# Performance work log

Measured on AMD Instinct MI355X. Metric: run time of the kernel, lower is better.

Reference implementation:

```python
import jax, jax.numpy as jnp
import numpy as np
import math

B, T, D, H = 2, 2048, 768, 12
ND = D // H  # head dim = 64


def precompute_freqs_cis(dim, end, theta=10000.0):
    freqs = 1.0 / (theta ** (jnp.arange(0, dim, 2, dtype=jnp.float32) / dim))  # [dim/2]
    t = jnp.arange(end, dtype=jnp.float32)
    freqs = jnp.outer(t, freqs)  # [end, dim/2]
    return jnp.cos(freqs), jnp.sin(freqs)


def apply_rotary_emb(q, k, cos, sin):
    # q, k: [b, t, h, nd]; cos/sin: [t, nd/2]
    def rot(x):
        xr, xi = x[..., 0::2], x[..., 1::2]  # even/odd interleaved split
        c = cos[None, :, None, :]
        s = sin[None, :, None, :]
        out_r = xr * c - xi * s
        out_i = xr * s + xi * c
        return jnp.stack([out_r, out_i], axis=-1).reshape(x.shape)
    return rot(q), rot(k)


def setup_inputs() -> dict:
    key = jax.random.key(0)
    ks = jax.random.split(key, 12)
    sc = 0.02
    q = jax.random.normal(ks[0], (B, T, D), dtype=jnp.float32)
    k = jax.random.normal(ks[1], (B, T, D), dtype=jnp.float32)
    v = jax.random.normal(ks[2], (B, T, D), dtype=jnp.float32)
    mask = jnp.tril(jnp.ones((T, T), dtype=jnp.int32))[None, None]  # causal [1,1,T,T]
    # weights stored as [d_in, d_out] (pre-transposed vs torch Linear)
    wq = jax.random.normal(ks[3], (D, D), dtype=jnp.float32) * sc
    bq = jax.random.normal(ks[4], (D,), dtype=jnp.float32) * sc
    wk = jax.random.normal(ks[5], (D, D), dtype=jnp.float32) * sc
    bk = jax.random.normal(ks[6], (D,), dtype=jnp.float32) * sc
    wv = jax.random.normal(ks[7], (D, D), dtype=jnp.float32) * sc
    bv = jax.random.normal(ks[8], (D,), dtype=jnp.float32) * sc
    wo = jax.random.normal(ks[9], (D, D), dtype=jnp.float32) * sc
    cos, sin = precompute_freqs_cis(ND, T)
    return {"q": q, "k": k, "v": v, "mask": mask, "wq": wq, "bq": bq,
            "wk": wk, "bk": bk, "wv": wv, "bv": bv, "wo": wo,
            "freqs_cos": cos, "freqs_sin": sin}


def reference(q, k, v, mask, wq, bq, wk, bk, wv, bv, wo, freqs_cos, freqs_sin):
    b, t, d = q.shape
    qh = (q @ wq + bq).reshape(b, t, H, ND)
    kh = (k @ wk + bk).reshape(b, t, H, ND)
    vh = (v @ wv + bv).reshape(b, t, H, ND).transpose(0, 2, 1, 3)  # [b,h,t,nd]
    qh, kh = apply_rotary_emb(qh, kh, freqs_cos[:t], freqs_sin[:t])
    qh = qh.transpose(0, 2, 1, 3)  # [b,h,t,nd]
    kh = kh.transpose(0, 2, 1, 3)
    attn = jnp.einsum('bhqd,bhkd->bhqk', qh, kh) / math.sqrt(ND)
    attn = jnp.where(mask == 0, jnp.float32(-jnp.inf), attn)
    probs = jax.nn.softmax(attn, axis=-1)
    out = jnp.einsum('bhqk,bhkd->bhqd', probs, vh)
    out = out.transpose(0, 2, 1, 3).reshape(b, t, d)
    return out @ wo
```

## Files before the change

kernel.cpp:

```cpp
#include <hip/hip_runtime.h>
#include <hip/hip_bf16.h>
#include <math.h>

#define BB 2
#define TT 2048
#define DD 768
#define HH 12
#define ND 64
#define MM (BB*TT)

typedef __attribute__((ext_vector_type(8))) short bf16x8;
typedef __attribute__((ext_vector_type(4))) float f32x4;
typedef __attribute__((ext_vector_type(16))) float f32x16;

__device__ __forceinline__ float bf2f(ushort u) {
    union { unsigned int i; float f; } v; v.i = ((unsigned int)u) << 16; return v.f;
}
__device__ __forceinline__ ushort f2bf(float f) {
    union { float f; unsigned int i; } v; v.f = f;
    unsigned int r = v.i + 0x7FFF + ((v.i >> 16) & 1);
    return (ushort)(r >> 16);
}

__device__ __forceinline__ void cp16(void* lds, const void* g) {
    __builtin_amdgcn_global_load_lds(
        (const __attribute__((address_space(1))) void*)g,
        (__attribute__((address_space(3))) void*)lds, 16, 0, 0);
}

__device__ __forceinline__ float fexp2(float x) {
    float r; asm("v_exp_f32 %0, %1" : "=v"(r) : "v"(x)); return r;
}
__device__ __forceinline__ unsigned int pk_bf16(float a, float b) {
    unsigned int r; asm("v_cvt_pk_bf16_f32 %0, %1, %2" : "=v"(r) : "v"(a), "v"(b)); return r;
}

__device__ __forceinline__ void plswap(unsigned int& a, unsigned int& b) {
#if __has_builtin(__builtin_amdgcn_permlane32_swap)
    auto r = __builtin_amdgcn_permlane32_swap(a, b, false, false);
    a = r[0]; b = r[1];
#else
    unsigned int sa = __shfl_xor((int)a, 32), sb = __shfl_xor((int)b, 32);
    bool hi = (threadIdx.x & 63) >= 32;
    unsigned int na = hi ? sb : a, nb = hi ? b : sa;
    a = na; b = nb;
#endif
}
__device__ __forceinline__ float partner32(float x, int hi) {
#if __has_builtin(__builtin_amdgcn_permlane32_swap)
    unsigned int u = __float_as_uint(x);
    auto r = __builtin_amdgcn_permlane32_swap(u, u, false, false);
    return __uint_as_float(hi ? r[0] : r[1]);
#else
    return __shfl_xor(x, 32);
#endif
}

#define QSCALE 0.18033688011112043f

__global__ void conv_x3(const float* __restrict__ x0, const float* __restrict__ x1,
                        const float* __restrict__ x2,
                        ushort* __restrict__ o0, ushort* __restrict__ o1,
                        ushort* __restrict__ o2)
{
    const float* x = blockIdx.z == 0 ? x0 : (blockIdx.z == 1 ? x1 : x2);
    ushort* o = blockIdx.z == 0 ? o0 : (blockIdx.z == 1 ? o1 : o2);
    int i = (blockIdx.x * 256 + threadIdx.x) * 4;
    if (i >= MM * DD) return;
    float4 v = *(const float4*)&x[i];
    ushort4 r;
    r.x = f2bf(v.x); r.y = f2bf(v.y); r.z = f2bf(v.z); r.w = f2bf(v.w);
    *(ushort4*)&o[i] = r;
}

__global__ __launch_bounds__(256) void conv_wT(const float* __restrict__ w0, const float* __restrict__ w1,
                        const float* __restrict__ w2, const float* __restrict__ w3,
                        ushort* __restrict__ o0, ushort* __restrict__ o1,
                        ushort* __restrict__ o2, ushort* __restrict__ o3)
{
    __shared__ ushort tile[64][72];
    const float* w = blockIdx.z == 0 ? w0 : blockIdx.z == 1 ? w1 : blockIdx.z == 2 ? w2 : w3;
    ushort* o = blockIdx.z == 0 ? o0 : blockIdx.z == 1 ? o1 : blockIdx.z == 2 ? o2 : o3;
    const int k0 = blockIdx.y * 64, n0 = blockIdx.x * 64;
    #pragma unroll
    for (int it = 0; it < 4; ++it) {
        int e = (threadIdx.x + it * 256) * 4;
        int r = e >> 6, c = e & 63;
        float4 v = *(const float4*)&w[(size_t)(k0 + r) * DD + n0 + c];
        tile[c + 0][r] = f2bf(v.x);
        tile[c + 1][r] = f2bf(v.y);
        tile[c + 2][r] = f2bf(v.z);
        tile[c + 3][r] = f2bf(v.w);
    }
    __syncthreads();
    #pragma unroll
    for (int it = 0; it < 4; ++it) {
        int e = (threadIdx.x + it * 256) * 4;
        int nr = e >> 6, kc = e & 63;
        ushort4 r4;
        r4.x = tile[nr][kc + 0];
        r4.y = tile[nr][kc + 1];
        r4.z = tile[nr][kc + 2];
        r4.w = tile[nr][kc + 3];
        *(ushort4*)&o[(size_t)(n0 + nr) * DD + k0 + kc] = r4;
    }
}

struct GArgs { const ushort* x; const ushort* wt; const float* bias; void* out;
               const float* cT; const float* sT; int rope; };

template<int MODE, int TM, int TN>
__global__ __launch_bounds__(256) void gemm_bf16(GArgs a0, GArgs a1, GArgs a2)
{
    constexpr int WM = TM / 2, WN = TN / 2;
    constexpr int MF = WM / 16, NF = WN / 16;
    constexpr int BUFB = (TM + TN) * 64;
    constexpr int NPASS = BUFB / 4096;
    __shared__ __align__(16) ushort S[2][BUFB / 2];
    GArgs ga = (blockIdx.z == 0) ? a0 : (blockIdx.z == 1 ? a1 : a2);
    const int tid = threadIdx.x;
    const int w = tid >> 6, l = tid & 63;
    const int wr = w >> 1, wc = w & 1;
    const int n0 = blockIdx.x * TN, m0 = blockIdx.y * TM;

    f32x4 acc[MF][NF] = {};

    auto stage = [&](int buf, int k0) {
        #pragma unroll
        for (int it = 0; it < NPASS; ++it) {
            const int ob = it * 4096 + w * 1024;
            const int o = ob + l * 16;
            if (ob < TM * 64) {
                const int row = o >> 6, kb = o & 63;
                cp16((char*)&S[buf][0] + ob,
                     (const char*)ga.x + (size_t)(m0 + row) * (DD * 2) + k0 * 2 + kb);
            } else {
                const int o2 = o - TM * 64;
                const int row = o2 >> 6, kb = o2 & 63;
                cp16((char*)&S[buf][0] + ob,
                     (const char*)ga.wt + (size_t)(n0 + row) * (DD * 2) + k0 * 2 + kb);
            }
        }
    };
    stage(0, 0);
    __syncthreads();
    const int NK = DD / 32;
    for (int t = 0; t < NK; ++t) {
        const int cur = t & 1;
        if (t + 1 < NK) stage(cur ^ 1, (t + 1) * 32);
        const char* ab = (const char*)&S[cur][0];
        bf16x8 af[MF], bfr[NF];
        #pragma unroll
        for (int i = 0; i < MF; ++i)
            af[i] = *(const bf16x8*)(ab + (WM * wr + 16 * i + (l & 15)) * 64 + (l >> 4) * 16);
        #pragma unroll
        for (int j = 0; j < NF; ++j)
            bfr[j] = *(const bf16x8*)(ab + TM * 64 + (WN * wc + 16 * j + (l & 15)) * 64 + (l >> 4) * 16);
        #pragma unroll
        for (int i = 0; i < MF; ++i)
            #pragma unroll
            for (int j = 0; j < NF; ++j)
                acc[i][j] = __builtin_amdgcn_mfma_f32_16x16x32_bf16(af[i], bfr[j], acc[i][j], 0, 0, 0);
        __syncthreads();
    }
    #pragma unroll
    for (int i = 0; i < MF; ++i) {
        #pragma unroll
        for (int j = 0; j < NF; ++j) {
            #pragma unroll
            for (int r = 0; r < 4; ++r) {
                const int m = m0 + WM * wr + 16 * i + (l >> 4) * 4 + r;
                const int n = n0 + WN * wc + 16 * j + (l & 15);
                float v = acc[i][j][r];
                if (MODE == 0) {
                    v += ga.bias[n];
                    const int tt = m & 2047;
                    if (ga.rope) {
                        const int d = n & 63;
                        const float c = ga.cT[tt * 32 + (d >> 1)];
                        const float s = ga.sT[tt * 32 + (d >> 1)];
                        const float p = __shfl_xor(v, 1);
                        v = (n & 1) ? (p * s + v * c) : (v * c - p * s);
                        if (ga.rope == 2) v *= QSCALE;
                    }
                    const int b = m >> 11;
                    const int h = n >> 6, d = n & 63;
                    ((ushort*)ga.out)[((size_t)(b * HH + h) * TT + tt) * ND + d] = f2bf(v);
                } else {
                    ((float*)ga.out)[(size_t)m * DD + n] = v;
                }
            }
        }
    }
}

__global__ __launch_bounds__(256) void transpose_v(const ushort* __restrict__ Vh,
                                                   ushort* __restrict__ VhT)
{
    __shared__ ushort tile[64][72];
    const int t0 = blockIdx.x * 64, bh = blockIdx.y;
    const ushort* src = Vh + ((size_t)bh * TT + t0) * ND;
    #pragma unroll
    for (int it = 0; it < 4; ++it) {
        int e = (threadIdx.x + it * 256) * 4;
        int r = e >> 6, c = e & 63;
        ushort4 v = *(const ushort4*)&src[r * ND + c];
        tile[r][c + 0] = v.x; tile[r][c + 1] = v.y;
        tile[r][c + 2] = v.z; tile[r][c + 3] = v.w;
    }
    __syncthreads();
    #pragma unroll
    for (int it = 0; it < 4; ++it) {
        int e = (threadIdx.x + it * 256) * 4;
        int d = e >> 6, tc = e & 63;
        ushort4 r4;
        r4.x = tile[tc + 0][d]; r4.y = tile[tc + 1][d];
        r4.z = tile[tc + 2][d]; r4.w = tile[tc + 3][d];
        *(ushort4*)&VhT[((size_t)bh * ND + d) * TT + t0 + tc] = r4;
    }
}

#define NQB (TT/128)
#define NBH (BB*HH)
#define NTASK (NQB*NBH)
#define NCU 256

__global__ __launch_bounds__(512) void attn_mfma4(const ushort* __restrict__ Qh,
                                                  const ushort* __restrict__ Kh,
                                                  const ushort* __restrict__ VhT,
                                                  ushort* __restrict__ Op)
{
    __shared__ __align__(16) ushort Ks[2][2][4096];
    __shared__ __align__(16) ushort Vs[2][2][4096];
    const int tid = threadIdx.x;
    const int w = tid >> 6, l = tid & 63;
    const int lq = l & 31, hi = l >> 5;
    const int qs = w & 3;
    const int kvh = w >> 2;

    const int n = blockIdx.x;
    const int r_ = (n < NCU) ? n : (NTASK - 1 + NCU - n);
    const int qblk = (NQB - 1) - r_ / NBH;
    const int bh = r_ % NBH;

    const int q0 = qblk * 128;
    const int q0w = q0 + qs * 32;
    const int qg = q0w + lq;
    const int ntH = qblk + 1;
    const int kvbase = kvh * ntH * 64;

    const ushort* Qg = Qh + ((size_t)bh * TT + q0w) * ND;
    const ushort* Kg = Kh + (size_t)bh * TT * ND;
    const ushort* Vg = VhT + (size_t)bh * ND * TT;

    bf16x8 qf[4];
    #pragma unroll
    for (int ks = 0; ks < 4; ++ks)
        qf[ks] = *(const bf16x8*)((const char*)Qg + lq * 128 + ks * 32 + hi * 16);

    auto stageKV = [&](int buf, int kv0) {
        #pragma unroll
        for (int it = 0; it < 2; ++it) {
            int o = it * 4096 + qs * 1024 + l * 16;
            int row = o >> 7, inner = o & 127;
            int swz = inner ^ ((row & 7) << 4);
            cp16((char*)&Ks[kvh][buf][0] + it * 4096 + qs * 1024,
                 (const char*)Kg + (size_t)(kv0 + row) * 128 + swz);
            cp16((char*)&Vs[kvh][buf][0] + it * 4096 + qs * 1024,
                 (const char*)Vg + (size_t)row * (TT * 2) + kv0 * 2 + swz);
        }
    };

    float m = -1e30f, lsum = 0.f;
    f32x16 o0 = {}, o1 = {};

    stageKV(0, kvbase);
    __syncthreads();
    for (int t = 0; t < ntH; ++t) {
        const int cur = t & 1;
        if (t + 1 < ntH) stageKV(cur ^ 1, kvbase + (t + 1) * 64);
        const char* kb = (const char*)&Ks[kvh][cur][0];
        const char* vb = (const char*)&Vs[kvh][cur][0];
        const int kvt = kvbase + t * 64;

        if (kvt <= q0w + 31) {
            const bool have1 = (kvt + 32 <= q0w + 31);

            f32x16 st0 = {}, st1 = {};
            __builtin_amdgcn_s_setprio(1);
            #pragma unroll
            for (int ks = 0; ks < 4; ++ks) {
                bf16x8 kf = *(const bf16x8*)(kb + lq * 128 +
                                             ((ks * 32 + hi * 16) ^ ((lq & 7) << 4)));
                st0 = __builtin_amdgcn_mfma_f32_32x32x16_bf16(kf, qf[ks], st0, 0, 0, 0);
            }
            if (have1) {
                #pragma unroll
                for (int ks = 0; ks < 4; ++ks) {
                    bf16x8 kf = *(const bf16x8*)(kb + (32 + lq) * 128 +
                                                 ((ks * 32 + hi * 16) ^ ((lq & 7) << 4)));
                    st1 = __builtin_amdgcn_mfma_f32_32x32x16_bf16(kf, qf[ks], st1, 0, 0, 0);
                }
            }
            __builtin_amdgcn_s_setprio(0);

            float tm = -1e30f;
            if (kvt + 31 > q0w) {
                #pragma unroll
                for (int r = 0; r < 16; ++r) {
                    const int kvg = kvt + (r & 3) + 8 * (r >> 2) + 4 * hi;
                    float x = (kvg <= qg) ? st0[r] : -1e30f;
                    st0[r] = x;
                    tm = fmaxf(tm, x);
                }
            } else {
                #pragma unroll
                for (int r = 0; r < 16; ++r) tm = fmaxf(tm, st0[r]);
            }
            if (have1) {
                if (kvt + 63 > q0w) {
                    #pragma unroll
                    for (int r = 0; r < 16; ++r) {
                        const int kvg = kvt + 32 + (r & 3) + 8 * (r >> 2) + 4 * hi;
                        float x = (kvg <= qg) ? st1[r] : -1e30f;
                        st1[r] = x;
                        tm = fmaxf(tm, x);
                    }
                } else {
                    #pragma unroll
                    for (int r = 0; r < 16; ++r) tm = fmaxf(tm, st1[r]);
                }
            }
            tm = fmaxf(tm, partner32(tm, hi));

            const bool defer = __all(tm <= m + 11.5f);
            float alpha = 1.f;
            if (!defer) {
                const float nm = fmaxf(m, tm);
                alpha = fexp2(m - nm);
                m = nm;
            }

            float ps[16];
            unsigned int pkA[8], pkB[8];
            #pragma unroll
            for (int i = 0; i < 8; ++i) {
                const float p0 = fexp2(st0[2 * i + 0] - m);
                const float p1 = fexp2(st0[2 * i + 1] - m);
                pkA[i] = pk_bf16(p0, p1);
                ps[i] = p0 + p1;
            }
            if (have1) {
                #pragma unroll
                for (int i = 0; i < 8; ++i) {
                    const float p0 = fexp2(st1[2 * i + 0] - m);
                    const float p1 = fexp2(st1[2 * i + 1] - m);
                    pkB[i] = pk_bf16(p0, p1);
                    ps[8 + i] = p0 + p1;
                }
            } else {
                #pragma unroll
                for (int i = 0; i < 8; ++i) { pkB[i] = 0; ps[8 + i] = 0.f; }
            }
            const float t0s = (ps[0] + ps[1]) + (ps[2] + ps[3]);
            const float t1s = (ps[4] + ps[5]) + (ps[6] + ps[7]);
            const float t2s = (ps[8] + ps[9]) + (ps[10] + ps[11]);
            const float t3s = (ps[12] + ps[13]) + (ps[14] + ps[15]);
            float rs = (t0s + t1s) + (t2s + t3s);
            rs += partner32(rs, hi);
            lsum = lsum * alpha + rs;

            plswap(pkA[0], pkA[2]); plswap(pkA[1], pkA[3]);
            plswap(pkA[4], pkA[6]); plswap(pkA[5], pkA[7]);
            if (have1) {
                plswap(pkB[0], pkB[2]); plswap(pkB[1], pkB[3]);
                plswap(pkB[4], pkB[6]); plswap(pkB[5], pkB[7]);
            }
            union { unsigned int u[4]; bf16x8 v; } pa0, pa1, pa2, pa3;
            pa0.u[0] = pkA[0]; pa0.u[1] = pkA[1]; pa0.u[2] = pkA[2]; pa0.u[3] = pkA[3];
            pa1.u[0] = pkA[4]; pa1.u[1] = pkA[5]; pa1.u[2] = pkA[6]; pa1.u[3] = pkA[7];
            pa2.u[0] = pkB[0]; pa2.u[1] = pkB[1]; pa2.u[2] = pkB[2]; pa2.u[3] = pkB[3];
            pa3.u[0] = pkB[4]; pa3.u[1] = pkB[5]; pa3.u[2] = pkB[6]; pa3.u[3] = pkB[7];

            if (!defer) {
                #pragma unroll
                for (int r = 0; r < 16; ++r) { o0[r] *= alpha; o1[r] *= alpha; }
            }

            __builtin_amdgcn_s_setprio(1);
            #pragma unroll
            for (int sl = 0; sl < 2; ++sl) {
                const bf16x8 pf = sl == 0 ? pa0.v : pa1.v;
                const int cb = sl * 32 + hi * 16;
                bf16x8 va = *(const bf16x8*)(vb + lq * 128 + (cb ^ ((lq & 7) << 4)));
                bf16x8 vc = *(const bf16x8*)(vb + (lq + 32) * 128 + (cb ^ ((lq & 7) << 4)));
                o0 = __builtin_amdgcn_mfma_f32_32x32x16_bf16(va, pf, o0, 0, 0, 0);
                o1 = __builtin_amdgcn_mfma_f32_32x32x16_bf16(vc, pf, o1, 0, 0, 0);
            }
            if (have1) {
                #pragma unroll
                for (int sl = 0; sl < 2; ++sl) {
                    const bf16x8 pf = sl == 0 ? pa2.v : pa3.v;
                    const int cb = 64 + sl * 32 + hi * 16;
                    bf16x8 va = *(const bf16x8*)(vb + lq * 128 + (cb ^ ((lq & 7) << 4)));
                    bf16x8 vc = *(const bf16x8*)(vb + (lq + 32) * 128 + (cb ^ ((lq & 7) << 4)));
                    o0 = __builtin_amdgcn_mfma_f32_32x32x16_bf16(va, pf, o0, 0, 0, 0);
                    o1 = __builtin_amdgcn_mfma_f32_32x32x16_bf16(vc, pf, o1, 0, 0, 0);
                }
            }
            __builtin_amdgcn_s_setprio(0);
        }
        __syncthreads();
    }

    float* xO  = (float*)&Ks[0][0][0];
    float* xML = (float*)&Vs[0][0][0];
    if (kvh == 1) {
        float* dst = xO + qs * 2048;
        #pragma unroll
        for (int r = 0; r < 16; ++r) {
            dst[r * 64 + l] = o0[r];
            dst[(r + 16) * 64 + l] = o1[r];
        }
        if (hi == 0) { xML[qs * 64 + lq] = m; xML[qs * 64 + 32 + lq] = lsum; }
    }
    __syncthreads();
    if (kvh == 0) {
        const float* src = xO + qs * 2048;
        const float m1 = xML[qs * 64 + lq];
        const float l1 = xML[qs * 64 + 32 + lq];
        const float ms = fmaxf(m, m1);
        const float a0 = fexp2(m - ms), a1 = fexp2(m1 - ms);
        const float inv = 1.0f / (lsum * a0 + l1 * a1);
        const int b = bh / HH, h = bh % HH;
        ushort* dst = Op + ((size_t)(b * TT + qg)) * DD + h * ND;
        #pragma unroll
        for (int g = 0; g < 4; ++g) {
            ushort4 w0, w1;
            w0.x = f2bf((o0[4 * g + 0] * a0 + src[(4 * g + 0) * 64 + l] * a1) * inv);
            w0.y = f2bf((o0[4 * g + 1] * a0 + src[(4 * g + 1) * 64 + l] * a1) * inv);
            w0.z = f2bf((o0[4 * g + 2] * a0 + src[(4 * g + 2) * 64 + l] * a1) * inv);
            w0.w = f2bf((o0[4 * g + 3] * a0 + src[(4 * g + 3) * 64 + l] * a1) * inv);
            *(ushort4*)&dst[8 * g + 4 * hi] = w0;
            w1.x = f2bf((o1[4 * g + 0] * a0 + src[(16 + 4 * g + 0) * 64 + l] * a1) * inv);
            w1.y = f2bf((o1[4 * g + 1] * a0 + src[(16 + 4 * g + 1) * 64 + l] * a1) * inv);
            w1.z = f2bf((o1[4 * g + 2] * a0 + src[(16 + 4 * g + 2) * 64 + l] * a1) * inv);
            w1.w = f2bf((o1[4 * g + 3] * a0 + src[(16 + 4 * g + 3) * 64 + l] * a1) * inv);
            *(ushort4*)&dst[32 + 8 * g + 4 * hi] = w1;
        }
    }
}

extern "C" void kernel_launch(void* const* d_in, const int* in_sizes, int n_in,
                              void* d_out, int out_size, void* d_ws, size_t ws_size,
                              hipStream_t stream)
{
    const float* q  = (const float*)d_in[0];
    const float* k  = (const float*)d_in[1];
    const float* v  = (const float*)d_in[2];
    const float* wq = (const float*)d_in[4];
    const float* bq = (const float*)d_in[5];
    const float* wk = (const float*)d_in[6];
    const float* bk = (const float*)d_in[7];
    const float* wv = (const float*)d_in[8];
    const float* bv = (const float*)d_in[9];
    const float* wo = (const float*)d_in[10];
    const float* fc = (const float*)d_in[11];
    const float* fs = (const float*)d_in[12];
    float* out = (float*)d_out;

    ushort* qB  = (ushort*)d_ws;
    ushort* kB  = qB  + (size_t)MM * DD;
    ushort* vB  = kB  + (size_t)MM * DD;
    ushort* wqT = vB  + (size_t)MM * DD;
    ushort* wkT = wqT + (size_t)DD * DD;
    ushort* wvT = wkT + (size_t)DD * DD;
    ushort* woT = wvT + (size_t)DD * DD;
    ushort* Qh  = woT + (size_t)DD * DD;
    ushort* Kh  = Qh  + (size_t)MM * DD;
    ushort* Vh  = Kh  + (size_t)MM * DD;
    ushort* VhT = kB;
    ushort* Op  = qB;

    conv_x3<<<dim3(MM * DD / 4 / 256, 1, 3), 256, 0, stream>>>(q, k, v, qB, kB, vB);
    conv_wT<<<dim3(DD / 64, DD / 64, 4), 256, 0, stream>>>(wq, wk, wv, wo, wqT, wkT, wvT, woT);

    GArgs aq{qB, wqT, bq, (void*)Qh, fc, fs, 2};
    GArgs ak{kB, wkT, bk, (void*)Kh, fc, fs, 1};
    GArgs av{vB, wvT, bv, (void*)Vh, nullptr, nullptr, 0};
    gemm_bf16<0, 128, 64><<<dim3(DD / 64, MM / 128, 3), 256, 0, stream>>>(aq, ak, av);

    transpose_v<<<dim3(TT / 64, BB * HH), 256, 0, stream>>>(Vh, VhT);

    attn_mfma4<<<dim3(NTASK), 512, 0, stream>>>(Qh, Kh, VhT, Op);

    GArgs ao{Op, woT, nullptr, (void*)out, nullptr, nullptr, 0};
    gemm_bf16<1, 64, 64><<<dim3(DD / 64, MM / 64, 1), 256, 0, stream>>>(ao, ao, ao);
}
```

Measured before the change: 108.4 us.

## Triple-buffer GEMM staging with vmcnt waits and XCD-aware block remap

The GEMM moves from double to triple-buffered LDS staging, keeping two K-tiles in flight. It replaces __syncthreads with explicit vmcnt waits plus raw barriers, and raises wave priority around the MFMA block. A 1D grid is remapped so consecutive tasks land on the same XCD (8-way interleave), aiming for better L2 reuse. The cost is more LDS per block and hand-counted vmcnt values that must match the number of outstanding async copies.

```diff
diff --git a/kernel.cpp b/kernel.cpp
--- a/kernel.cpp
+++ b/kernel.cpp
@@ -110,18 +110,27 @@
                const float* cT; const float* sT; int rope; };
 
 template<int MODE, int TM, int TN>
-__global__ __launch_bounds__(256) void gemm_bf16(GArgs a0, GArgs a1, GArgs a2)
+__global__ __launch_bounds__(256) void gemm_bf16(GArgs a0, GArgs a1, GArgs a2,
+                                                 int nx, int ny)
 {
     constexpr int WM = TM / 2, WN = TN / 2;
     constexpr int MF = WM / 16, NF = WN / 16;
     constexpr int BUFB = (TM + TN) * 64;
     constexpr int NPASS = BUFB / 4096;
-    __shared__ __align__(16) ushort S[2][BUFB / 2];
-    GArgs ga = (blockIdx.z == 0) ? a0 : (blockIdx.z == 1 ? a1 : a2);
+    constexpr int NK = DD / 32;
+    __shared__ __align__(16) ushort S[3][BUFB / 2];
     const int tid = threadIdx.x;
     const int w = tid >> 6, l = tid & 63;
     const int wr = w >> 1, wc = w & 1;
-    const int n0 = blockIdx.x * TN, m0 = blockIdx.y * TM;
+
+    const int G = gridDim.x, per = G >> 3;
+    const int p = blockIdx.x;
+    const int task = (p & 7) * per + (p >> 3);
+    const int bx = task % nx;
+    const int by = (task / nx) % ny;
+    const int bz = task / (nx * ny);
+    GArgs ga = (bz == 0) ? a0 : (bz == 1 ? a1 : a2);
+    const int n0 = bx * TN, m0 = by * TM;
 
     f32x4 acc[MF][NF] = {};
 
@@ -142,13 +151,18 @@
             }
         }
     };
+
     stage(0, 0);
-    __syncthreads();
-    const int NK = DD / 32;
+    stage(1, 32);
+    if constexpr (NPASS == 2) asm volatile("s_waitcnt vmcnt(2)" ::: "memory");
+    else                      asm volatile("s_waitcnt vmcnt(3)" ::: "memory");
+    __builtin_amdgcn_s_barrier();
+
     for (int t = 0; t < NK; ++t) {
-        const int cur = t & 1;
-        if (t + 1 < NK) stage(cur ^ 1, (t + 1) * 32);
-        const char* ab = (const char*)&S[cur][0];
+        const bool more = (t + 2 < NK);
+        if (more) stage((t + 2) % 3, (t + 2) * 32);
+
+        const char* ab = (const char*)&S[t % 3][0];
         bf16x8 af[MF], bfr[NF];
         #pragma unroll
         for (int i = 0; i < MF; ++i)
@@ -156,13 +170,24 @@
         #pragma unroll
         for (int j = 0; j < NF; ++j)
             bfr[j] = *(const bf16x8*)(ab + TM * 64 + (WN * wc + 16 * j + (l & 15)) * 64 + (l >> 4) * 16);
+        __builtin_amdgcn_s_setprio(1);
         #pragma unroll
         for (int i = 0; i < MF; ++i)
             #pragma unroll
             for (int j = 0; j < NF; ++j)
                 acc[i][j] = __builtin_amdgcn_mfma_f32_16x16x32_bf16(af[i], bfr[j], acc[i][j], 0, 0, 0);
-        __syncthreads();
-    }
+        __builtin_amdgcn_s_setprio(0);
+
+        if (more) {
+            if constexpr (NPASS == 2) asm volatile("s_waitcnt vmcnt(2)" ::: "memory");
+            else                      asm volatile("s_waitcnt vmcnt(3)" ::: "memory");
+        } else {
+            asm volatile("s_waitcnt vmcnt(0)" ::: "memory");
+        }
+        __builtin_amdgcn_s_barrier();
+    }
+    asm volatile("s_waitcnt vmcnt(0)" ::: "memory");
+
     #pragma unroll
     for (int i = 0; i < MF; ++i) {
         #pragma unroll
@@ -179,8 +204,8 @@
                         const int d = n & 63;
                         const float c = ga.cT[tt * 32 + (d >> 1)];
                         const float s = ga.sT[tt * 32 + (d >> 1)];
-                        const float p = __shfl_xor(v, 1);
-                        v = (n & 1) ? (p * s + v * c) : (v * c - p * s);
+                        const float pv = __shfl_xor(v, 1);
+                        v = (n & 1) ? (pv * s + v * c) : (v * c - pv * s);
                         if (ga.rope == 2) v *= QSCALE;
                     }
                     const int b = m >> 11;
@@ -488,12 +513,12 @@
     GArgs aq{qB, wqT, bq, (void*)Qh, fc, fs, 2};
     GArgs ak{kB, wkT, bk, (void*)Kh, fc, fs, 1};
     GArgs av{vB, wvT, bv, (void*)Vh, nullptr, nullptr, 0};
-    gemm_bf16<0, 128, 64><<<dim3(DD / 64, MM / 128, 3), 256, 0, stream>>>(aq, ak, av);
+    gemm_bf16<0, 128, 64><<<dim3(1152), 256, 0, stream>>>(aq, ak, av, DD / 64, MM / 128);
 
     transpose_v<<<dim3(TT / 64, BB * HH), 256, 0, stream>>>(Vh, VhT);
 
     attn_mfma4<<<dim3(NTASK), 512, 0, stream>>>(Qh, Kh, VhT, Op);
 
     GArgs ao{Op, woT, nullptr, (void*)out, nullptr, nullptr, 0};
-    gemm_bf16<1, 64, 64><<<dim3(DD / 64, MM / 64, 1), 256, 0, stream>>>(ao, ao, ao);
-}
+    gemm_bf16<1, 64, 64><<<dim3(768), 256, 0, stream>>>(ao, ao, ao, DD / 64, MM / 64);
+}
```

Measured after the change: 109.8 us. Within noise of the previous version (+1.3%).

## Double GEMM K-tile to 64 with XOR-swizzled LDS layout and MFMA priority

Applied to the files above, without the earlier changes.

The bf16 GEMM now stages a 64-wide K slice per iteration instead of 32, halving the number of outer iterations and barriers. LDS rows become 128 bytes with an XOR swizzle on the 16-byte chunk index, applied on both the global-to-LDS copy and the fragment reads, to avoid bank conflicts. The MFMA block is wrapped in s_setprio to favour math issue. In exchange the kernel uses twice the LDS per block, which may lower occupancy.

```diff
diff --git a/kernel.cpp b/kernel.cpp
--- a/kernel.cpp
+++ b/kernel.cpp
@@ -114,8 +114,10 @@
 {
     constexpr int WM = TM / 2, WN = TN / 2;
     constexpr int MF = WM / 16, NF = WN / 16;
-    constexpr int BUFB = (TM + TN) * 64;
+    constexpr int ABYTES = TM * 128;
+    constexpr int BUFB = (TM + TN) * 128;
     constexpr int NPASS = BUFB / 4096;
+    constexpr int NK = DD / 64;
     __shared__ __align__(16) ushort S[2][BUFB / 2];
     GArgs ga = (blockIdx.z == 0) ? a0 : (blockIdx.z == 1 ? a1 : a2);
     const int tid = threadIdx.x;
@@ -130,39 +132,53 @@
         for (int it = 0; it < NPASS; ++it) {
             const int ob = it * 4096 + w * 1024;
             const int o = ob + l * 16;
-            if (ob < TM * 64) {
-                const int row = o >> 6, kb = o & 63;
+            if (ob < ABYTES) {
+                const int row = o >> 7, inner = o & 127;
                 cp16((char*)&S[buf][0] + ob,
-                     (const char*)ga.x + (size_t)(m0 + row) * (DD * 2) + k0 * 2 + kb);
+                     (const char*)ga.x + (size_t)(m0 + row) * (DD * 2) + k0 * 2 +
+                     (inner ^ ((row & 7) << 4)));
             } else {
-                const int o2 = o - TM * 64;
-                const int row = o2 >> 6, kb = o2 & 63;
+                const int o2 = o - ABYTES;
+                const int row = o2 >> 7, inner = o2 & 127;
                 cp16((char*)&S[buf][0] + ob,
-                     (const char*)ga.wt + (size_t)(n0 + row) * (DD * 2) + k0 * 2 + kb);
+                     (const char*)ga.wt + (size_t)(n0 + row) * (DD * 2) + k0 * 2 +
+                     (inner ^ ((row & 7) << 4)));
             }
         }
     };
+
     stage(0, 0);
     __syncthreads();
-    const int NK = DD / 32;
+    const int lq = l >> 4, lr = l & 15;
     for (int t = 0; t < NK; ++t) {
         const int cur = t & 1;
-        if (t + 1 < NK) stage(cur ^ 1, (t + 1) * 32);
+        if (t + 1 < NK) stage(cur ^ 1, (t + 1) * 64);
         const char* ab = (const char*)&S[cur][0];
-        bf16x8 af[MF], bfr[NF];
         #pragma unroll
-        for (int i = 0; i < MF; ++i)
-            af[i] = *(const bf16x8*)(ab + (WM * wr + 16 * i + (l & 15)) * 64 + (l >> 4) * 16);
-        #pragma unroll
-        for (int j = 0; j < NF; ++j)
-            bfr[j] = *(const bf16x8*)(ab + TM * 64 + (WN * wc + 16 * j + (l & 15)) * 64 + (l >> 4) * 16);
-        #pragma unroll
-        for (int i = 0; i < MF; ++i)
-            #pragma unroll
-            for (int j = 0; j < NF; ++j)
-                acc[i][j] = __builtin_amdgcn_mfma_f32_16x16x32_bf16(af[i], bfr[j], acc[i][j], 0, 0, 0);
+        for (int kc = 0; kc < 2; ++kc) {
+            const int kb = kc * 64 + lq * 16;
+            bf16x8 af[MF], bfr[NF];
+            #pragma unroll
+            for (int i = 0; i < MF; ++i) {
+                const int row = WM * wr + 16 * i + lr;
+                af[i] = *(const bf16x8*)(ab + row * 128 + (kb ^ ((row & 7) << 4)));
+            }
+            #pragma unroll
+            for (int j = 0; j < NF; ++j) {
+                const int row = WN * wc + 16 * j + lr;
+                bfr[j] = *(const bf16x8*)(ab + ABYTES + row * 128 + (kb ^ ((row & 7) << 4)));
+            }
+            __builtin_amdgcn_s_setprio(1);
+            #pragma unroll
+            for (int i = 0; i < MF; ++i)
+                #pragma unroll
+                for (int j = 0; j < NF; ++j)
+                    acc[i][j] = __builtin_amdgcn_mfma_f32_16x16x32_bf16(af[i], bfr[j], acc[i][j], 0, 0, 0);
+            __builtin_amdgcn_s_setprio(0);
+        }
         __syncthreads();
     }
+
     #pragma unroll
     for (int i = 0; i < MF; ++i) {
         #pragma unroll
@@ -179,8 +195,8 @@
                         const int d = n & 63;
                         const float c = ga.cT[tt * 32 + (d >> 1)];
                         const float s = ga.sT[tt * 32 + (d >> 1)];
-                        const float p = __shfl_xor(v, 1);
-                        v = (n & 1) ? (p * s + v * c) : (v * c - p * s);
+                        const float pv = __shfl_xor(v, 1);
+                        v = (n & 1) ? (pv * s + v * c) : (v * c - pv * s);
                         if (ga.rope == 2) v *= QSCALE;
                     }
                     const int b = m >> 11;
```

New measurement: 105.1 us. -3.0%, faster.
